# Performance work log

Hardware: AMD Instinct MI355X
Metric: run time of the kernel (lower is better)

Reference implementation:

```python
import jax, jax.numpy as jnp
import numpy as np

DIM = 512
HEADS = 8
DIM_HEAD = 64
INNER = HEADS * DIM_HEAD  # 512
SCALE = DIM_HEAD ** -0.5


def setup_inputs() -> dict:
    key = jax.random.key(0)
    k1, k2, k3, k4 = jax.random.split(key, 4)
    x = jax.random.normal(k1, (4, 2048, DIM), dtype=jnp.float32)
    # Dense(inner_dim*3, use_bias=False): weight [dim, 3*inner]
    w_qkv = jax.random.normal(k2, (DIM, 3 * INNER), dtype=jnp.float32) * (DIM ** -0.5)
    # to_out Dense(dim): weight [inner, dim] + bias [dim]
    w_out = jax.random.normal(k3, (INNER, DIM), dtype=jnp.float32) * (INNER ** -0.5)
    b_out = jax.random.normal(k4, (DIM,), dtype=jnp.float32) * 0.01
    return {"x": x, "w_qkv": w_qkv, "w_out": w_out, "b_out": b_out}


def reference(x, w_qkv, w_out, b_out):
    b, n, _ = x.shape
    qkv = x @ w_qkv                                  # [b, n, 3*inner]
    q, k, v = jnp.split(qkv, 3, axis=-1)             # each [b, n, inner]
    def to_heads(t):
        return t.reshape(b, n, HEADS, DIM_HEAD).transpose(0, 2, 1, 3)  # [b, h, n, d]
    q, k, v = map(to_heads, (q, k, v))
    dots = jnp.einsum('bhid,bhjd->bhij', q, k) * SCALE
    attn = jax.nn.softmax(dots, axis=-1)
    out = jnp.einsum('bhij,bhjd->bhid', attn, v)     # [b, h, n, d]
    out = out.transpose(0, 2, 1, 3).reshape(b, n, INNER)
    return out @ w_out + b_out                       # [b, n, dim]
```

## Files before the change

### kernel.cpp

```cpp
#include <hip/hip_runtime.h>
#include <stdint.h>

#define DIM    512
#define HEADS  8
#define DHEAD  64
#define SEQ    2048
#define BATCH  4
#define BH     (BATCH*HEADS)
#define MROWS  (BATCH*SEQ)
#define NQKV   (3*DIM)
#define QSCALE 0.18033688011112042f

typedef __bf16 bf16x8 __attribute__((ext_vector_type(8)));
typedef float  f32x4  __attribute__((ext_vector_type(4)));
typedef float  f32x16 __attribute__((ext_vector_type(16)));

typedef unsigned short u16;

#if __has_builtin(__builtin_amdgcn_exp2f)
#define EXP2(x) __builtin_amdgcn_exp2f(x)
#else
#define EXP2(x) exp2f(x)
#endif

__device__ __forceinline__ u16 f2bf(float f) {
    union { float f; uint32_t u; } v; v.f = f;
    uint32_t u = v.u;
    uint32_t r = (u + 0x7FFFu + ((u >> 16) & 1u)) >> 16;
    return (u16)r;
}
__device__ __forceinline__ float bf2f(u16 h) {
    union { uint32_t u; float f; } v; v.u = ((uint32_t)h) << 16;
    return v.f;
}
__device__ __forceinline__ uint32_t pk2bf(float a, float b) {
    union { float f; uint32_t u; } ua, ub; ua.f = a; ub.f = b;
#if __has_builtin(__builtin_amdgcn_perm)
    return __builtin_amdgcn_perm(ub.u + 0x8000u, ua.u + 0x8000u, 0x07060302u);
#else
    return ((ua.u + 0x8000u) >> 16) | ((ub.u + 0x8000u) & 0xFFFF0000u);
#endif
}

#define P32SWAP(x, y) asm("v_permlane32_swap_b32 %0, %1" : "+v"(x), "+v"(y))

__device__ __forceinline__ void async16(const void* g, u16* l) {
    __builtin_amdgcn_global_load_lds(
        (const __attribute__((address_space(1))) void*)g,
        (__attribute__((address_space(3))) void*)l, 16, 0, 0);
}

#define XBLKS (MROWS * DIM / 4 / 256)
#define WQT   ((DIM / 64) * (NQKV / 64))
#define WOT   ((DIM / 64) * (DIM / 64))
__global__ void prep(const void* __restrict__ x, const void* __restrict__ wq,
                     const void* __restrict__ wo, u16* __restrict__ xb,
                     u16* __restrict__ wtq, u16* __restrict__ wto,
                     int* __restrict__ flag) {
    __shared__ int cnt;
    __shared__ __align__(16) u16 tile[64][72];
    int tid = threadIdx.x;
    if (tid == 0) cnt = 0;
    __syncthreads();
    {
        u16 v = ((const u16*)x)[tid * 2];
        int e = (v >> 7) & 0xFF;
        atomicAdd(&cnt, (v == 0) || (e >= 100 && e <= 140));
    }
    __syncthreads();
    int isbf = (cnt >= 192);
    int b = blockIdx.x;
    if (b == 0 && tid == 0) *flag = isbf;

    if (b < XBLKS) {
        int i = b * 256 + tid;
        if (isbf) {
            ((uint2*)xb)[i] = ((const uint2*)x)[i];
        } else {
            float4 v = ((const float4*)x)[i];
            ushort4 o;
            o.x = f2bf(v.x); o.y = f2bf(v.y); o.z = f2bf(v.z); o.w = f2bf(v.w);
            ((ushort4*)xb)[i] = o;
        }
        return;
    }
    const void* W; u16* Wt; int N, tb;
    if (b < XBLKS + WQT) { W = wq; Wt = wtq; N = NQKV; tb = b - XBLKS; }
    else                 { W = wo; Wt = wto; N = DIM;  tb = b - XBLKS - WQT; }
    int tn = N / 64;
    int k0 = (tb / tn) * 64, n0 = (tb - (tb / tn) * tn) * 64;

#pragma unroll 4
    for (int it = 0; it < 16; ++it) {
        int idx = it * 256 + tid;
        int r = idx >> 6, c = idx & 63;
        u16 v = isbf ? ((const u16*)W)[(size_t)(k0 + r) * N + n0 + c]
                     : f2bf(((const float*)W)[(size_t)(k0 + r) * N + n0 + c]);
        tile[c][r] = v;
    }
    __syncthreads();
    {
        int n = tid >> 2, ks = (tid & 3) * 16;
        uint4 v0 = *(const uint4*)&tile[n][ks];
        uint4 v1 = *(const uint4*)&tile[n][ks + 8];
        *(uint4*)&Wt[(size_t)(n0 + n) * DIM + k0 + ks] = v0;
        *(uint4*)&Wt[(size_t)(n0 + n) * DIM + k0 + ks + 8] = v1;
    }
}

template<int KDIM, int TM, int TN>
__device__ __forceinline__ void gemm_lds_db(
        const u16* __restrict__ A, const u16* __restrict__ Bt,
        int m0, int n0, int tid, u16* As, u16* Bs,
        f32x4 (&acc)[TM / 32][TN / 32]) {
    int lane = tid & 63, ln = lane & 15, quad = lane >> 4, w = tid >> 6;
    int wm = (w >> 1) * (TM / 2), wn = (w & 1) * (TN / 2);

    auto stage = [&](int buf, int k0) {
#pragma unroll
        for (int ii = 0; ii < TM / 64; ++ii) {
            int r0 = (ii * 4 + w) * 16;
            int row = r0 + (lane >> 2);
            int seg = (lane & 3) ^ (row & 3);
            async16(A + (size_t)(m0 + row) * KDIM + k0 + seg * 8,
                    As + buf * TM * 32 + r0 * 32);
        }
#pragma unroll
        for (int ii = 0; ii < TN / 64; ++ii) {
            int r0 = (ii * 4 + w) * 16;
            int row = r0 + (lane >> 2);
            int seg = (lane & 3) ^ (row & 3);
            async16(Bt + (size_t)(n0 + row) * KDIM + k0 + seg * 8,
                    Bs + buf * TN * 32 + r0 * 32);
        }
    };

    stage(0, 0);
#pragma unroll 1
    for (int kk = 0; kk < KDIM / 32; ++kk) {
        __syncthreads();
        if (kk + 1 < KDIM / 32) stage((kk + 1) & 1, (kk + 1) * 32);
        const u16* Ac = As + (kk & 1) * TM * 32;
        const u16* Bc = Bs + (kk & 1) * TN * 32;
        bf16x8 a[TM / 32], b[TN / 32];
        int rseg = (quad ^ (ln & 3)) * 8;
#pragma unroll
        for (int i = 0; i < TM / 32; ++i)
            a[i] = *(const bf16x8*)(Ac + (wm + i * 16 + ln) * 32 + rseg);
#pragma unroll
        for (int j = 0; j < TN / 32; ++j)
            b[j] = *(const bf16x8*)(Bc + (wn + j * 16 + ln) * 32 + rseg);
#pragma unroll
        for (int i = 0; i < TM / 32; ++i)
#pragma unroll
            for (int j = 0; j < TN / 32; ++j)
                acc[i][j] = __builtin_amdgcn_mfma_f32_16x16x32_bf16(
                    a[i], b[j], acc[i][j], 0, 0, 0);
    }
}

__global__ __launch_bounds__(256, 3) void qkv_gemm(
        const u16* __restrict__ X, const u16* __restrict__ Wt,
        u16* __restrict__ Qt, u16* __restrict__ Kb, u16* __restrict__ Vt) {
    __shared__ __align__(16) u16 As[2 * 128 * 32];
    __shared__ __align__(16) u16 Bs[2 * 128 * 32];

    int tid  = threadIdx.x;
    int lane = tid & 63, ln = lane & 15, quad = lane >> 4, wid = tid >> 6;
    int m0 = blockIdx.x * 128, n0 = blockIdx.y * 128;
    int wm = (wid >> 1) * 64, wn = (wid & 1) * 64;

    f32x4 acc[4][4];
#pragma unroll
    for (int i = 0; i < 4; ++i)
#pragma unroll
        for (int j = 0; j < 4; ++j) acc[i][j] = 0.f;

    gemm_lds_db<DIM, 128, 128>(X, Wt, m0, n0, tid, As, Bs, acc);

#pragma unroll
    for (int j = 0; j < 4; ++j) {
        int col   = n0 + wn + j * 16 + ln;
        int which = col >> 9;
        int hd    = col & 511;
        int h     = hd >> 6, d = hd & 63;
#pragma unroll
        for (int i = 0; i < 4; ++i) {
            int rbase = m0 + wm + i * 16 + quad * 4;
            int b = rbase >> 11, n = rbase & 2047;
            int bh = b * HEADS + h;
            if (which == 1) {
#pragma unroll
                for (int r = 0; r < 4; ++r)
                    Kb[((size_t)bh * SEQ + n + r) * DHEAD + d] = f2bf(acc[i][j][r]);
            } else {
                float s = (which == 0) ? QSCALE : 1.0f;
                uint2 pv;
                pv.x = pk2bf(acc[i][j][0] * s, acc[i][j][1] * s);
                pv.y = pk2bf(acc[i][j][2] * s, acc[i][j][3] * s);
                u16* dst = (which == 0) ? Qt : Vt;
                *(uint2*)&dst[((size_t)bh * DHEAD + d) * SEQ + n] = pv;
            }
        }
    }
}

__global__ __launch_bounds__(256, 1) void flash_attn(
        const u16* __restrict__ Qt, const u16* __restrict__ Kb,
        const u16* __restrict__ Vt, u16* __restrict__ Ob) {
    __shared__ __align__(16) u16 Kc[2][64 * 64];
    __shared__ __align__(16) u16 Vc[2][64 * 64];

    int tid  = threadIdx.x;
    int lane = tid & 63, c = lane & 31, hi = lane >> 5, wid = tid >> 6;
    int bh = blockIdx.x;
    int q0 = blockIdx.y * 256 + wid * 64;

    const u16* Qh = Qt + (size_t)bh * SEQ * DHEAD;
    const u16* Kh = Kb + (size_t)bh * SEQ * DHEAD;
    const u16* Vh = Vt + (size_t)bh * DHEAD * SEQ;

    int srow = lane >> 3;
    auto stageKV = [&](int buf, int kc) {
#pragma unroll
        for (int ii = 0; ii < 2; ++ii) {
            int slab = wid + ii * 4;
            int g = (lane & 7) ^ srow ^ (slab & 3);
            const u16* gk = Kh + (size_t)(kc + slab * 8 + srow) * DHEAD + g * 8;
            async16(gk, &Kc[buf][slab * 8 * 64]);
            const u16* gv = Vh + (size_t)(slab * 8 + srow) * SEQ + kc + g * 8;
            async16(gv, &Vc[buf][slab * 8 * 64]);
        }
    };

    bf16x8 qf[2][4];
#pragma unroll
    for (int qg = 0; qg < 2; ++qg)
#pragma unroll
        for (int ds = 0; ds < 4; ++ds) {
            union { u16 a[8]; bf16x8 v; } u;
#pragma unroll
            for (int j = 0; j < 8; ++j)
                u.a[j] = Qh[(size_t)(ds * 16 + hi * 8 + j) * SEQ + q0 + qg * 32 + c];
            qf[qg][ds] = u.v;
        }

    bf16x8 onesf;
    { union { uint32_t d[4]; bf16x8 v; } u;
      u.d[0] = u.d[1] = u.d[2] = u.d[3] = 0x3F803F80u; onesf = u.v; }

    f32x16 o[2][2];
    f32x16 lacc[2];
#pragma unroll
    for (int qg = 0; qg < 2; ++qg) {
        lacc[qg] = 0.f;
#pragma unroll
        for (int dt = 0; dt < 2; ++dt) o[qg][dt] = 0.f;
    }

    stageKV(0, 0);
    __syncthreads();

    int fl = (c & 7) ^ ((c >> 3) & 3);

#pragma unroll 1
    for (int kc = 0; kc < SEQ; kc += 64) {
        int cur = (kc >> 6) & 1;
        if (kc + 64 < SEQ) stageKV(cur ^ 1, kc + 64);

#pragma unroll
        for (int kt = 0; kt < 2; ++kt) {
            bf16x8 kf[4];
#pragma unroll
            for (int ds = 0; ds < 4; ++ds) {
                int slot = (ds * 2 + hi) ^ fl;
                kf[ds] = *(const bf16x8*)&Kc[cur][(kt * 32 + c) * 64 + slot * 8];
            }

            bf16x8 pa[2][2];
#pragma unroll
            for (int qg = 0; qg < 2; ++qg) {
                f32x16 s;
                s = 0.f;
#pragma unroll
                for (int ds = 0; ds < 4; ++ds)
                    s = __builtin_amdgcn_mfma_f32_32x32x16_bf16(
                        kf[ds], qf[qg][ds], s, 0, 0, 0);
                float p[16];
#pragma unroll
                for (int r = 0; r < 16; ++r) p[r] = EXP2(s[r]);
                uint32_t X[8];
#pragma unroll
                for (int i = 0; i < 8; ++i) X[i] = pk2bf(p[2 * i], p[2 * i + 1]);
                P32SWAP(X[0], X[2]); P32SWAP(X[1], X[3]);
                P32SWAP(X[4], X[6]); P32SWAP(X[5], X[7]);
                union { uint32_t d[4]; bf16x8 v; } u0, u1;
                u0.d[0] = X[0]; u0.d[1] = X[1]; u0.d[2] = X[2]; u0.d[3] = X[3];
                u1.d[0] = X[4]; u1.d[1] = X[5]; u1.d[2] = X[6]; u1.d[3] = X[7];
                pa[qg][0] = u0.v; pa[qg][1] = u1.v;
            }

#pragma unroll
            for (int tl = 0; tl < 2; ++tl) {
#pragma unroll
                for (int dt = 0; dt < 2; ++dt) {
                    int slot = ((kt * 2 + tl) * 2 + hi) ^ fl;
                    bf16x8 vf = *(const bf16x8*)&Vc[cur][(dt * 32 + c) * 64 + slot * 8];
#pragma unroll
                    for (int qg = 0; qg < 2; ++qg)
                        o[qg][dt] = __builtin_amdgcn_mfma_f32_32x32x16_bf16(
                            pa[qg][tl], vf, o[qg][dt], 0, 0, 0);
                }
#pragma unroll
                for (int qg = 0; qg < 2; ++qg)
                    lacc[qg] = __builtin_amdgcn_mfma_f32_32x32x16_bf16(
                        pa[qg][tl], onesf, lacc[qg], 0, 0, 0);
            }
        }
        __syncthreads();
    }

    int b = bh >> 3, hh = bh & 7;
#pragma unroll
    for (int qg = 0; qg < 2; ++qg) {
        f32x16 linv;
#pragma unroll
        for (int r = 0; r < 16; ++r) linv[r] = 1.0f / lacc[qg][r];
#pragma unroll
        for (int dt = 0; dt < 2; ++dt)
#pragma unroll
            for (int r = 0; r < 16; ++r) {
                int ql = (r & 3) + 8 * (r >> 2) + 4 * hi;
                int n  = q0 + qg * 32 + ql;
                int d  = dt * 32 + c;
                Ob[((size_t)(b * SEQ + n)) * DIM + hh * DHEAD + d] =
                    f2bf(o[qg][dt][r] * linv[r]);
            }
    }
}

__global__ __launch_bounds__(256, 3) void out_gemm(
        const u16* __restrict__ A, const u16* __restrict__ Wt,
        const void* __restrict__ bias, void* __restrict__ out,
        const int* __restrict__ flag) {
    __shared__ __align__(16) u16 As[2 * 64 * 32];
    __shared__ __align__(16) u16 Bs[2 * 128 * 32];

    int tid  = threadIdx.x;
    int lane = tid & 63, ln = lane & 15, quad = lane >> 4, wid = tid >> 6;
    int m0 = blockIdx.x * 64, n0 = blockIdx.y * 128;
    int wm = (wid >> 1) * 32, wn = (wid & 1) * 64;
    int isbf = *flag;

    f32x4 acc[2][4];
#pragma unroll
    for (int i = 0; i < 2; ++i)
#pragma unroll
        for (int j = 0; j < 4; ++j) acc[i][j] = 0.f;

    gemm_lds_db<DIM, 64, 128>(A, Wt, m0, n0, tid, As, Bs, acc);

#pragma unroll
    for (int j = 0; j < 4; ++j) {
        int col = n0 + wn + j * 16 + ln;
        float bv = isbf ? bf2f(((const u16*)bias)[col])
                        : ((const float*)bias)[col];
#pragma unroll
        for (int i = 0; i < 2; ++i) {
            int rbase = m0 + wm + i * 16 + quad * 4;
#pragma unroll
            for (int r = 0; r < 4; ++r) {
                int row = rbase + r;
                size_t off = (size_t)row * DIM + col;
                float val = acc[i][j][r] + bv;
                if (isbf) ((u16*)out)[off] = f2bf(val);
                else      ((float*)out)[off] = val;
            }
        }
    }
}

extern "C" void kernel_launch(void* const* d_in, const int* in_sizes, int n_in,
                              void* d_out, int out_size, void* d_ws, size_t ws_size,
                              hipStream_t stream) {
    const void* x     = d_in[0];
    const void* w_qkv = d_in[1];
    const void* w_out = d_in[2];
    const void* b_out = d_in[3];

    int* flag   = (int*)d_ws;
    u16* x_bf   = (u16*)((char*)d_ws + 16);
    u16* wt_qkv = x_bf + (size_t)MROWS * DIM;
    u16* wt_out = wt_qkv + (size_t)NQKV * DIM;
    u16* Qt     = wt_out + (size_t)DIM * DIM;
    u16* Kb     = Qt + (size_t)BH * SEQ * DHEAD;
    u16* Vt     = Kb + (size_t)BH * SEQ * DHEAD;
    u16* attn   = x_bf;

    prep<<<XBLKS + WQT + WOT, 256, 0, stream>>>(
        x, w_qkv, w_out, x_bf, wt_qkv, wt_out, flag);
    qkv_gemm<<<dim3(MROWS / 128, NQKV / 128), 256, 0, stream>>>(x_bf, wt_qkv, Qt, Kb, Vt);
    flash_attn<<<dim3(BH, SEQ / 256), 256, 0, stream>>>(Qt, Kb, Vt, attn);
    out_gemm<<<dim3(MROWS / 64, DIM / 128), 256, 0, stream>>>(attn, wt_out, b_out, d_out, flag);
}
```

Baseline: 191.8 us.

## Halve flash-attention query tile per wave and add MFMA priority hints

Each wave now processes 32 query rows instead of 64, so blocks cover 128 queries and the grid doubles to 512 blocks. Launch bounds move to two blocks per CU so more waves are resident. s_setprio is raised around the MFMA sections to favour matrix issue over other waves. The cost is that each K/V tile staged in shared memory is reused across half as many queries, doubling K/V global and LDS traffic per unit of work.

```diff
diff --git a/kernel.cpp b/kernel.cpp
--- a/kernel.cpp
+++ b/kernel.cpp
@@ -205,7 +205,7 @@
     }
 }
 
-__global__ __launch_bounds__(256, 1) void flash_attn(
+__global__ __launch_bounds__(256, 2) void flash_attn(
         const u16* __restrict__ Qt, const u16* __restrict__ Kb,
         const u16* __restrict__ Vt, u16* __restrict__ Ob) {
     __shared__ __align__(16) u16 Kc[2][64 * 64];
@@ -214,7 +214,7 @@
     int tid  = threadIdx.x;
     int lane = tid & 63, c = lane & 31, hi = lane >> 5, wid = tid >> 6;
     int bh = blockIdx.x;
-    int q0 = blockIdx.y * 256 + wid * 64;
+    int q0 = blockIdx.y * 128 + wid * 32;
 
     const u16* Qh = Qt + (size_t)bh * SEQ * DHEAD;
     const u16* Kh = Kb + (size_t)bh * SEQ * DHEAD;
@@ -233,30 +233,25 @@
         }
     };
 
-    bf16x8 qf[2][4];
-#pragma unroll
-    for (int qg = 0; qg < 2; ++qg)
-#pragma unroll
-        for (int ds = 0; ds < 4; ++ds) {
-            union { u16 a[8]; bf16x8 v; } u;
-#pragma unroll
-            for (int j = 0; j < 8; ++j)
-                u.a[j] = Qh[(size_t)(ds * 16 + hi * 8 + j) * SEQ + q0 + qg * 32 + c];
-            qf[qg][ds] = u.v;
-        }
+    bf16x8 qf[4];
+#pragma unroll
+    for (int ds = 0; ds < 4; ++ds) {
+        union { u16 a[8]; bf16x8 v; } u;
+#pragma unroll
+        for (int j = 0; j < 8; ++j)
+            u.a[j] = Qh[(size_t)(ds * 16 + hi * 8 + j) * SEQ + q0 + c];
+        qf[ds] = u.v;
+    }
 
     bf16x8 onesf;
     { union { uint32_t d[4]; bf16x8 v; } u;
       u.d[0] = u.d[1] = u.d[2] = u.d[3] = 0x3F803F80u; onesf = u.v; }
 
-    f32x16 o[2][2];
-    f32x16 lacc[2];
-#pragma unroll
-    for (int qg = 0; qg < 2; ++qg) {
-        lacc[qg] = 0.f;
-#pragma unroll
-        for (int dt = 0; dt < 2; ++dt) o[qg][dt] = 0.f;
-    }
+    f32x16 o[2];
+    f32x16 lacc;
+    lacc = 0.f;
+#pragma unroll
+    for (int dt = 0; dt < 2; ++dt) o[dt] = 0.f;
 
     stageKV(0, 0);
     __syncthreads();
@@ -277,66 +272,61 @@
                 kf[ds] = *(const bf16x8*)&Kc[cur][(kt * 32 + c) * 64 + slot * 8];
             }
 
-            bf16x8 pa[2][2];
-#pragma unroll
-            for (int qg = 0; qg < 2; ++qg) {
-                f32x16 s;
-                s = 0.f;
-#pragma unroll
-                for (int ds = 0; ds < 4; ++ds)
-                    s = __builtin_amdgcn_mfma_f32_32x32x16_bf16(
-                        kf[ds], qf[qg][ds], s, 0, 0, 0);
-                float p[16];
-#pragma unroll
-                for (int r = 0; r < 16; ++r) p[r] = EXP2(s[r]);
-                uint32_t X[8];
-#pragma unroll
-                for (int i = 0; i < 8; ++i) X[i] = pk2bf(p[2 * i], p[2 * i + 1]);
-                P32SWAP(X[0], X[2]); P32SWAP(X[1], X[3]);
-                P32SWAP(X[4], X[6]); P32SWAP(X[5], X[7]);
-                union { uint32_t d[4]; bf16x8 v; } u0, u1;
-                u0.d[0] = X[0]; u0.d[1] = X[1]; u0.d[2] = X[2]; u0.d[3] = X[3];
-                u1.d[0] = X[4]; u1.d[1] = X[5]; u1.d[2] = X[6]; u1.d[3] = X[7];
-                pa[qg][0] = u0.v; pa[qg][1] = u1.v;
-            }
-
+            f32x16 s;
+            s = 0.f;
+            __builtin_amdgcn_s_setprio(1);
+#pragma unroll
+            for (int ds = 0; ds < 4; ++ds)
+                s = __builtin_amdgcn_mfma_f32_32x32x16_bf16(
+                    kf[ds], qf[ds], s, 0, 0, 0);
+            __builtin_amdgcn_s_setprio(0);
+
+            float p[16];
+#pragma unroll
+            for (int r = 0; r < 16; ++r) p[r] = EXP2(s[r]);
+            uint32_t X[8];
+#pragma unroll
+            for (int i = 0; i < 8; ++i) X[i] = pk2bf(p[2 * i], p[2 * i + 1]);
+            P32SWAP(X[0], X[2]); P32SWAP(X[1], X[3]);
+            P32SWAP(X[4], X[6]); P32SWAP(X[5], X[7]);
+            bf16x8 pa[2];
+            union { uint32_t d[4]; bf16x8 v; } u0, u1;
+            u0.d[0] = X[0]; u0.d[1] = X[1]; u0.d[2] = X[2]; u0.d[3] = X[3];
+            u1.d[0] = X[4]; u1.d[1] = X[5]; u1.d[2] = X[6]; u1.d[3] = X[7];
+            pa[0] = u0.v; pa[1] = u1.v;
+
+            __builtin_amdgcn_s_setprio(1);
 #pragma unroll
             for (int tl = 0; tl < 2; ++tl) {
 #pragma unroll
                 for (int dt = 0; dt < 2; ++dt) {
                     int slot = ((kt * 2 + tl) * 2 + hi) ^ fl;
                     bf16x8 vf = *(const bf16x8*)&Vc[cur][(dt * 32 + c) * 64 + slot * 8];
-#pragma unroll
-                    for (int qg = 0; qg < 2; ++qg)
-                        o[qg][dt] = __builtin_amdgcn_mfma_f32_32x32x16_bf16(
-                            pa[qg][tl], vf, o[qg][dt], 0, 0, 0);
+                    o[dt] = __builtin_amdgcn_mfma_f32_32x32x16_bf16(
+                        pa[tl], vf, o[dt], 0, 0, 0);
                 }
-#pragma unroll
-                for (int qg = 0; qg < 2; ++qg)
-                    lacc[qg] = __builtin_amdgcn_mfma_f32_32x32x16_bf16(
-                        pa[qg][tl], onesf, lacc[qg], 0, 0, 0);
+                lacc = __builtin_amdgcn_mfma_f32_32x32x16_bf16(
+                    pa[tl], onesf, lacc, 0, 0, 0);
             }
+            __builtin_amdgcn_s_setprio(0);
         }
         __syncthreads();
     }
 
     int b = bh >> 3, hh = bh & 7;
-#pragma unroll
-    for (int qg = 0; qg < 2; ++qg) {
-        f32x16 linv;
-#pragma unroll
-        for (int r = 0; r < 16; ++r) linv[r] = 1.0f / lacc[qg][r];
-#pragma unroll
-        for (int dt = 0; dt < 2; ++dt)
-#pragma unroll
-            for (int r = 0; r < 16; ++r) {
-                int ql = (r & 3) + 8 * (r >> 2) + 4 * hi;
-                int n  = q0 + qg * 32 + ql;
-                int d  = dt * 32 + c;
-                Ob[((size_t)(b * SEQ + n)) * DIM + hh * DHEAD + d] =
-                    f2bf(o[qg][dt][r] * linv[r]);
-            }
-    }
+    f32x16 linv;
+#pragma unroll
+    for (int r = 0; r < 16; ++r) linv[r] = 1.0f / lacc[r];
+#pragma unroll
+    for (int dt = 0; dt < 2; ++dt)
+#pragma unroll
+        for (int r = 0; r < 16; ++r) {
+            int ql = (r & 3) + 8 * (r >> 2) + 4 * hi;
+            int n  = q0 + ql;
+            int d  = dt * 32 + c;
+            Ob[((size_t)(b * SEQ + n)) * DIM + hh * DHEAD + d] =
+                f2bf(o[dt][r] * linv[r]);
+        }
 }
 
 __global__ __launch_bounds__(256, 3) void out_gemm(
@@ -400,6 +390,6 @@
     prep<<<XBLKS + WQT + WOT, 256, 0, stream>>>(
         x, w_qkv, w_out, x_bf, wt_qkv, wt_out, flag);
     qkv_gemm<<<dim3(MROWS / 128, NQKV / 128), 256, 0, stream>>>(x_bf, wt_qkv, Qt, Kb, Vt);
-    flash_attn<<<dim3(BH, SEQ / 256), 256, 0, stream>>>(Qt, Kb, Vt, attn);
+    flash_attn<<<dim3(BH, SEQ / 128), 256, 0, stream>>>(Qt, Kb, Vt, attn);
     out_gemm<<<dim3(MROWS / 64, DIM / 128), 256, 0, stream>>>(attn, wt_out, b_out, d_out, flag);
 }
```

After: 174.4 us. 9.1% less time.
